# Optimization experiments

Measured on AMD Instinct MI355X. Metric: run time of the kernel, lower is better.

Reference implementation:

```python
import jax, jax.numpy as jnp
import numpy as np

SPATIAL = [(56, 100), (28, 50), (14, 25), (7, 13)]
L_TOT = sum(h * w for h, w in SPATIAL)  # 7441
IMG_H, IMG_W = 448.0, 800.0
HH, NLEV, NPTS = 8, 4, 4
C, FFN = 256, 1024
PC = [-54.0, -54.0, -5.0, 54.0, 54.0, 3.0]
GRID_XY = 1080 // 8


def mlp2(x, w1, b1, w2, b2):
    return jnp.maximum(x @ w1 + b1, 0.0) @ w2 + b2


def ln(x):
    m = x.mean(-1, keepdims=True)
    v = ((x - m) ** 2).mean(-1, keepdims=True)
    return (x - m) * jax.lax.rsqrt(v + 1e-5)


def bilinear_sample(feat, loc):
    # feat [h,w,D]; loc [N,2] normalized to [0,1]; zero padding, align_corners=False
    h, w = feat.shape[0], feat.shape[1]
    x = loc[:, 0] * w - 0.5
    y = loc[:, 1] * h - 0.5
    x0f = jnp.floor(x); y0f = jnp.floor(y)
    wx = (x - x0f)[:, None]; wy = (y - y0f)[:, None]
    x0 = x0f.astype(jnp.int32); y0 = y0f.astype(jnp.int32)
    def g(xi, yi):
        inb = ((xi >= 0) & (xi < w) & (yi >= 0) & (yi < h))[:, None]
        return feat[jnp.clip(yi, 0, h - 1), jnp.clip(xi, 0, w - 1)] * inb
    return (g(x0, y0) * (1 - wx) * (1 - wy) + g(x0 + 1, y0) * wx * (1 - wy)
            + g(x0, y0 + 1) * (1 - wx) * wy + g(x0 + 1, y0 + 1) * wx * wy)


def setup_inputs() -> dict:
    key = jax.random.key(0)
    ks = jax.random.split(key, 40)
    B, V, P = 4, 6, 200
    f = jnp.float32
    def w(i, shape, s=0.05):
        return jax.random.normal(ks[i], shape, f) * s
    inp = {
        'img_query_feat': jax.random.normal(ks[1], (B, C, P), f),
        'img_query_pos': jax.random.uniform(ks[2], (B, P, 3), dtype=f),
        'img_query_view_mask': jax.random.randint(ks[3], (B, P, V), 0, 2).astype(jnp.int32),
        'img_feats_stack': jax.random.normal(ks[4], (B, V, C, L_TOT), f),
        'normal_img_feats_pos_stack': jax.random.normal(ks[5], (L_TOT, 2), f),
        'lidar2img_rt': jnp.eye(4, dtype=f) + 0.01 * jax.random.normal(ks[0], (B, V, 4, 4), f),
        'lidar2cam_r': jnp.broadcast_to(jnp.eye(3, dtype=f), (B, V, 3, 3)) + 0.01 * jax.random.normal(ks[6], (B, V, 3, 3), f),
        'lidar2cam_t': jax.random.normal(ks[7], (B, V, 3), f),
        'qpos_w1': w(8, (3, C)), 'qpos_b1': jnp.zeros((C,), f),
        'qpos_w2': w(9, (C, C)), 'qpos_b2': jnp.zeros((C,), f),
        'kpos_w1': w(10, (6, C)), 'kpos_b1': jnp.zeros((C,), f),
        'kpos_w2': w(11, (C, C)), 'kpos_b2': jnp.zeros((C,), f),
        'sa_wq': w(12, (C, C)), 'sa_wk': w(13, (C, C)),
        'sa_wv': w(14, (C, C)), 'sa_wo': w(15, (C, C)),
        'dv_w': w(16, (C, C)),
        'doff_w': w(17, (C, HH * NLEV * NPTS * 2)), 'doff_b': jnp.zeros((HH * NLEV * NPTS * 2,), f),
        'dattn_w': w(18, (C, HH * NLEV * NPTS)), 'dattn_b': jnp.zeros((HH * NLEV * NPTS,), f),
        'dout_w': w(19, (C, C)),
        'ffn_w1': w(20, (C, FFN)), 'ffn_b1': jnp.zeros((FFN,), f),
        'ffn_w2': w(21, (FFN, C)), 'ffn_b2': jnp.zeros((C,), f),
        'pred_w1': w(22, (C, C)), 'pred_b1': jnp.zeros((C,), f),
        'pred_w2': w(23, (C, 3)), 'pred_b2': jnp.zeros((3,), f),
    }
    return inp


def reference(img_query_feat, img_query_pos, img_query_view_mask, img_feats_stack,
              normal_img_feats_pos_stack, lidar2img_rt, lidar2cam_r, lidar2cam_t,
              qpos_w1, qpos_b1, qpos_w2, qpos_b2, kpos_w1, kpos_b1, kpos_w2, kpos_b2,
              sa_wq, sa_wk, sa_wv, sa_wo, dv_w, doff_w, doff_b, dattn_w, dattn_b, dout_w,
              ffn_w1, ffn_b1, ffn_w2, ffn_b2, pred_w1, pred_b1, pred_w2, pred_b2):
    B, V, _, L = img_feats_stack.shape
    P = img_query_feat.shape[-1]
    Dh = C // HH

    # key 3D positions: denormalize -> backproject via inv(lidar2img) -> append cam center
    pos2d = jax.nn.sigmoid(normal_img_feats_pos_stack) * jnp.array([IMG_W, IMG_H], jnp.float32)
    pos4 = jnp.concatenate([pos2d, jnp.ones((L, 2), pos2d.dtype)], -1)  # [L,4]
    inv_rt = jnp.linalg.inv(lidar2img_rt)                               # [B,V,4,4]
    key3d = jnp.einsum('bvij,lj->bvli', inv_rt, pos4)[..., :3]          # [B,V,L,3]
    cam_t = -jnp.einsum('bvji,bvj->bvi', lidar2cam_r, lidar2cam_t)      # [B,V,3]
    key_pos6 = jnp.concatenate([key3d, jnp.broadcast_to(cam_t[:, :, None], key3d.shape)], -1)
    kpos_emb = mlp2(key_pos6, kpos_w1, kpos_b1, kpos_w2, kpos_b2)       # [B,V,L,C]
    qpos_emb = mlp2(img_query_pos, qpos_w1, qpos_b1, qpos_w2, qpos_b2)  # [B,P,C]

    # per-view normalized reference points from lidar->image projection
    qpad = jnp.concatenate([img_query_pos, jnp.ones((B, P, 1), img_query_pos.dtype)], -1)
    proj = jnp.einsum('bvij,bpj->bvpi', lidar2img_rt, qpad)
    ref = (proj[..., :2] / proj[..., 2:3]) / jnp.array([IMG_W, IMG_H], jnp.float32)  # [B,V,P,2]

    # on-image mask; views with <=1 query are skipped (as in original)
    mv = jnp.transpose(img_query_view_mask > 0, (0, 2, 1))  # [B,V,P]
    mv = mv & (mv.sum(-1, keepdims=True) > 1)

    # self attention among on-image queries (shared qkv, per-view key mask)
    x = jnp.transpose(img_query_feat, (0, 2, 1))  # [B,P,C]
    xq = x + qpos_emb
    q = (xq @ sa_wq).reshape(B, P, HH, Dh)
    k = (xq @ sa_wk).reshape(B, P, HH, Dh)
    v = (x @ sa_wv).reshape(B, P, HH, Dh)
    logits = jnp.einsum('bqhd,bkhd->bhqk', q, k) / np.sqrt(Dh).astype(np.float32)
    logits = logits[:, None] + jnp.where(mv[:, :, None, None, :], 0.0, -1e9)  # [B,V,HH,P,P]
    attn = jax.nn.softmax(logits, axis=-1)
    sa = jnp.einsum('bvhqk,bkhd->bvqhd', attn, v).reshape(B, V, P, C) @ sa_wo
    x1 = ln(x[:, None] + sa)  # [B,V,P,C]

    # multi-scale deformable cross attention
    vals = ((jnp.transpose(img_feats_stack, (0, 1, 3, 2)) + kpos_emb) @ dv_w).reshape(B, V, L, HH, Dh)
    q2 = x1 + qpos_emb[:, None]
    off = (q2 @ doff_w + doff_b).reshape(B, V, P, HH, NLEV, NPTS, 2)
    aw = jax.nn.softmax((q2 @ dattn_w + dattn_b).reshape(B, V, P, HH, NLEV * NPTS), -1)
    aw = aw.reshape(B, V, P, HH, NLEV, NPTS)
    wh = jnp.array([[float(w_), float(h_)] for (h_, w_) in SPATIAL], jnp.float32)  # [NLEV,2]
    loc = ref[:, :, :, None, None, None, :] + off / wh[:, None, :]
    out = jnp.zeros((B, V, P, HH, Dh), x.dtype)
    start = 0
    for l, (h_, w_) in enumerate(SPATIAL):
        feat_l = vals[:, :, start:start + h_ * w_]
        start += h_ * w_
        feat_l = jnp.transpose(feat_l.reshape(B, V, h_, w_, HH, Dh), (0, 1, 4, 2, 3, 5)).reshape(B * V * HH, h_, w_, Dh)
        loc_l = jnp.transpose(loc[:, :, :, :, l], (0, 1, 3, 2, 4, 5)).reshape(B * V * HH, P * NPTS, 2)
        s = jax.vmap(bilinear_sample)(feat_l, loc_l).reshape(B, V, HH, P, NPTS, Dh)
        out = out + jnp.einsum('bvhpnd,bvphn->bvphd', s, aw[:, :, :, :, l])
    x2 = ln(x1 + out.reshape(B, V, P, C) @ dout_w)
    x3 = ln(x2 + mlp2(x2, ffn_w1, ffn_b1, ffn_w2, ffn_b2))  # [B,V,P,C]

    # masked scatter-accumulate across views, count-normalized
    mk = mv[..., None].astype(x.dtype)            # [B,V,P,1]
    fused = (x3 * mk).sum(1) / (mk.sum(1) + 1e-4)  # [B,P,C]
    img_query_feat_out = jnp.transpose(fused, (0, 2, 1))

    # prediction head: center refinement + BEV normalization
    center = mlp2(fused, pred_w1, pred_b1, pred_w2, pred_b2) + img_query_pos  # [B,P,3]
    img_query_pos_out = jax.lax.stop_gradient(center)
    cx = (center[..., 0] - PC[0]) / (PC[3] - PC[0]) * GRID_XY
    cy = (center[..., 1] - PC[1]) / (PC[4] - PC[1]) * GRID_XY
    center_bev = jnp.stack([cx, cy], -1)
    img_query_pos_bev = jax.lax.stop_gradient(center_bev)
    height = jnp.transpose(center[..., 2:3], (0, 2, 1))
    center_out = jnp.transpose(center_bev, (0, 2, 1))
    return img_query_feat_out, img_query_pos_out, img_query_pos_bev, center_out, height
```

## Files before the change

### kernel.cpp

```cpp
#include <hip/hip_runtime.h>
#include <hip/hip_bf16.h>
#include <cstdint>
#include <cstddef>

using bf16 = __hip_bfloat16;
#define DEVFN static __device__ __forceinline__

constexpr int B = 4, V = 6, P = 200, C = 256, HH = 8, Dh = 32, NLEV = 4, NPTS = 4, FFN = 1024;
constexpr int L = 7441;
constexpr int BV = B * V, BP = B * P, BVP = B * V * P, BVL = B * V * L;
constexpr float IMG_W = 800.f, IMG_H = 448.f;

__constant__ int cLH[4] = {56, 28, 14, 7};
__constant__ int cLW[4] = {100, 50, 25, 13};
__constant__ int cLS[4] = {0, 5600, 7000, 7350};

constexpr size_t IRT   = 0;
constexpr size_t CAMT  = IRT + (size_t)BV * 16;
constexpr size_t MFLAG = CAMT + (size_t)BV * 3;
constexpr size_t Xo    = MFLAG + BV;
constexpr size_t QPOSo = Xo + (size_t)BP * C;
constexpr size_t Qo    = QPOSo + (size_t)BP * C;
constexpr size_t Ko    = Qo + (size_t)BP * C;
constexpr size_t VVo   = Ko + (size_t)BP * C;
constexpr size_t LOGo  = VVo + (size_t)BP * C;
constexpr size_t SAo   = LOGo + (size_t)B * HH * P * P;
constexpr size_t X1o   = SAo + (size_t)BVP * C;
constexpr size_t REFo  = X1o + (size_t)BVP * C;
constexpr size_t OFFo  = REFo + (size_t)BVP * 2;
constexpr size_t AWo   = OFFo + (size_t)BVP * 256;
constexpr size_t OUTSo = AWo + (size_t)BVP * 128;
constexpr size_t X2o   = OUTSo + (size_t)BVP * C;
constexpr size_t X3o   = X2o + (size_t)BVP * C;
constexpr size_t FUSEDo= X3o + (size_t)BVP * C;
constexpr size_t WS_FLOATS = FUSEDo + (size_t)BP * C;
constexpr size_t VALS_BYTE_OFF = ((WS_FLOATS * 4 + 255) / 256) * 256;
constexpr size_t VALS_ELEMS = (size_t)BVL * C;

constexpr size_t KW2T_O  = 0;
constexpr size_t DVWT_O  = 65536;
constexpr size_t WOT_O   = 131072;
constexpr size_t DOUTT_O = 196608;
constexpr size_t OAWT_O  = 262144;
constexpr size_t QKVT_O  = 360448;
constexpr size_t W1T_O   = 753664;
constexpr size_t W2T_O   = 1015808;
constexpr size_t HIDB_O  = 1277952;

constexpr size_t O0 = 0;
constexpr size_t O1 = O0 + (size_t)B * C * P;
constexpr size_t O2 = O1 + (size_t)B * P * 3;
constexpr size_t O3 = O2 + (size_t)B * P * 2;
constexpr size_t O4 = O3 + (size_t)B * 2 * P;

DEVFN float tof(bf16 x) { return __bfloat162float(x); }
DEVFN bf16  tobf(float x) { return __float2bfloat16(x); }

typedef __attribute__((ext_vector_type(8))) short short8;
typedef __attribute__((ext_vector_type(4))) float floatx4;

DEVFN float blockReduceSum(float v, float* red) {
    int j = threadIdx.x;
    __syncthreads();
    red[j] = v; __syncthreads();
    for (int s = 128; s > 0; s >>= 1) { if (j < s) red[j] += red[j + s]; __syncthreads(); }
    return red[0];
}
DEVFN float blockReduceMax(float v, float* red) {
    int j = threadIdx.x;
    __syncthreads();
    red[j] = v; __syncthreads();
    for (int s = 128; s > 0; s >>= 1) { if (j < s) red[j] = fmaxf(red[j], red[j + s]); __syncthreads(); }
    return red[0];
}

DEVFN float dotK(const float* __restrict__ s, const float* __restrict__ W, int j, int N, int K) {
    float acc = 0.f;
    for (int k = 0; k < K; k += 4) {
        float4 h = *(const float4*)(s + k);
        acc += h.x * W[(size_t)(k + 0) * N + j];
        acc += h.y * W[(size_t)(k + 1) * N + j];
        acc += h.z * W[(size_t)(k + 2) * N + j];
        acc += h.w * W[(size_t)(k + 3) * N + j];
    }
    return acc;
}

__global__ __launch_bounds__(64) void k_setup(const float* rt, const float* l2cr, const float* l2ct,
                                              const int* maskin, float* ws) {
    int t = threadIdx.x;
    if (t >= BV) return;
    float m[16], inv[16];
    for (int i = 0; i < 16; i++) m[i] = rt[t * 16 + i];
    inv[0]  =  m[5]*m[10]*m[15] - m[5]*m[11]*m[14] - m[9]*m[6]*m[15] + m[9]*m[7]*m[14] + m[13]*m[6]*m[11] - m[13]*m[7]*m[10];
    inv[4]  = -m[4]*m[10]*m[15] + m[4]*m[11]*m[14] + m[8]*m[6]*m[15] - m[8]*m[7]*m[14] - m[12]*m[6]*m[11] + m[12]*m[7]*m[10];
    inv[8]  =  m[4]*m[9]*m[15]  - m[4]*m[11]*m[13] - m[8]*m[5]*m[15] + m[8]*m[7]*m[13] + m[12]*m[5]*m[11] - m[12]*m[7]*m[9];
    inv[12] = -m[4]*m[9]*m[14]  + m[4]*m[10]*m[13] + m[8]*m[5]*m[14] - m[8]*m[6]*m[13] - m[12]*m[5]*m[10] + m[12]*m[6]*m[9];
    inv[1]  = -m[1]*m[10]*m[15] + m[1]*m[11]*m[14] + m[9]*m[2]*m[15] - m[9]*m[3]*m[14] - m[13]*m[2]*m[11] + m[13]*m[3]*m[10];
    inv[5]  =  m[0]*m[10]*m[15] - m[0]*m[11]*m[14] - m[8]*m[2]*m[15] + m[8]*m[3]*m[14] + m[12]*m[2]*m[11] - m[12]*m[3]*m[10];
    inv[9]  = -m[0]*m[9]*m[15]  + m[0]*m[11]*m[13] + m[8]*m[1]*m[15] - m[8]*m[3]*m[13] - m[12]*m[1]*m[11] + m[12]*m[3]*m[9];
    inv[13] =  m[0]*m[9]*m[14]  - m[0]*m[10]*m[13] - m[8]*m[1]*m[14] + m[8]*m[2]*m[13] + m[12]*m[1]*m[10] - m[12]*m[2]*m[9];
    inv[2]  =  m[1]*m[6]*m[15]  - m[1]*m[7]*m[14]  - m[5]*m[2]*m[15] + m[5]*m[3]*m[14] + m[13]*m[2]*m[7]  - m[13]*m[3]*m[6];
    inv[6]  = -m[0]*m[6]*m[15]  + m[0]*m[7]*m[14]  + m[4]*m[2]*m[15] - m[4]*m[3]*m[14] - m[12]*m[2]*m[7]  + m[12]*m[3]*m[6];
    inv[10] =  m[0]*m[5]*m[15]  - m[0]*m[7]*m[13]  - m[4]*m[1]*m[15] + m[4]*m[3]*m[13] + m[12]*m[1]*m[7]  - m[12]*m[3]*m[5];
    inv[14] = -m[0]*m[5]*m[14]  + m[0]*m[6]*m[13]  + m[4]*m[1]*m[14] - m[4]*m[2]*m[13] - m[12]*m[1]*m[6]  + m[12]*m[2]*m[5];
    inv[3]  = -m[1]*m[6]*m[11]  + m[1]*m[7]*m[10]  + m[5]*m[2]*m[11] - m[5]*m[3]*m[10] - m[9]*m[2]*m[7]   + m[9]*m[3]*m[6];
    inv[7]  =  m[0]*m[6]*m[11]  - m[0]*m[7]*m[10]  - m[4]*m[2]*m[11] + m[4]*m[3]*m[10] + m[8]*m[2]*m[7]   - m[8]*m[3]*m[6];
    inv[11] = -m[0]*m[5]*m[11]  + m[0]*m[7]*m[9]   + m[4]*m[1]*m[11] - m[4]*m[3]*m[9]  - m[8]*m[1]*m[7]   + m[8]*m[3]*m[5];
    inv[15] =  m[0]*m[5]*m[10]  - m[0]*m[6]*m[9]   - m[4]*m[1]*m[10] + m[4]*m[2]*m[9]  + m[8]*m[1]*m[6]   - m[8]*m[2]*m[5];
    float det = m[0]*inv[0] + m[1]*inv[4] + m[2]*inv[8] + m[3]*inv[12];
    float rd = 1.f / det;
    for (int i = 0; i < 16; i++) ws[IRT + t * 16 + i] = inv[i] * rd;
    float r9[9], tv[3];
    for (int i = 0; i < 9; i++) r9[i] = l2cr[t * 9 + i];
    for (int i = 0; i < 3; i++) tv[i] = l2ct[t * 3 + i];
    for (int i = 0; i < 3; i++)
        ws[CAMT + t * 3 + i] = -(r9[0 * 3 + i] * tv[0] + r9[1 * 3 + i] * tv[1] + r9[2 * 3 + i] * tv[2]);
    int b = t / V, v = t % V, cnt = 0;
    for (int p = 0; p < P; p++) cnt += (maskin[(b * P + p) * V + v] > 0) ? 1 : 0;
    ws[MFLAG + t] = (cnt > 1) ? 1.f : 0.f;
}

__global__ __launch_bounds__(256) void k_wprep_all(
        const float* kw2, const float* dvw, const float* wo, const float* dw,
        const float* offw, const float* attw, const float* wq, const float* wk, const float* wv,
        const float* w1, const float* w2, bf16* wb) {
    int bid = blockIdx.x, t = threadIdx.x;
    if (bid < 1024) {
        int reg = bid >> 8, n = bid & 255;
        const float* src = (reg == 0) ? kw2 : (reg == 1) ? dvw : (reg == 2) ? wo : dw;
        wb[(size_t)reg * 65536 + (size_t)n * 256 + t] = tobf(src[(size_t)t * 256 + n]);
    } else if (bid < 1408) {
        int n = bid - 1024;
        float v = (n < 256) ? offw[(size_t)t * 256 + n] : attw[(size_t)t * 128 + (n - 256)];
        wb[OAWT_O + (size_t)n * 256 + t] = tobf(v);
    } else if (bid < 2176) {
        int n = bid - 1408;
        bf16* dst = wb + QKVT_O + (size_t)n * 512;
        float v0 = (n < 256) ? wq[(size_t)t * 256 + n] : (n < 512) ? wk[(size_t)t * 256 + (n - 256)]
                                                                   : wv[(size_t)t * 256 + (n - 512)];
        dst[t] = tobf(v0);
        float v1 = (n < 256) ? wq[(size_t)t * 256 + n] : (n < 512) ? wk[(size_t)t * 256 + (n - 256)] : 0.f;
        dst[t + 256] = tobf(v1);
    } else if (bid < 3200) {
        int n = bid - 2176;
        wb[W1T_O + (size_t)n * 256 + t] = tobf(w1[(size_t)t * 1024 + n]);
    } else {
        int n = bid - 3200;
        bf16* dst = wb + W2T_O + (size_t)n * 1024;
        for (int kk = 0; kk < 4; kk++)
            dst[t + kk * 256] = tobf(w2[(size_t)(t + kk * 256) * 256 + n]);
    }
}

__global__ __launch_bounds__(256) void k_qpos(const float* qfeat, const float* qposin,
                                              const float* w1, const float* b1, const float* w2, const float* b2,
                                              float* ws) {
    int row = blockIdx.x, j = threadIdx.x;
    int b = row / P, p = row % P;
    __shared__ __align__(16) float pos[4];
    __shared__ __align__(16) float hid[C];
    if (j < 3) pos[j] = qposin[row * 3 + j];
    __syncthreads();
    float h = b1[j] + pos[0] * w1[0 * C + j] + pos[1] * w1[1 * C + j] + pos[2] * w1[2 * C + j];
    hid[j] = fmaxf(h, 0.f);
    __syncthreads();
    float acc = b2[j] + dotK(hid, w2, j, C, C);
    ws[QPOSo + (size_t)row * C + j] = acc;
    ws[Xo + (size_t)row * C + j] = qfeat[((size_t)b * C + j) * P + p];
}

constexpr int AST2 = 520;
__global__ __launch_bounds__(256) void k_qkv_mfma(const bf16* __restrict__ qkvT, float* ws) {
    __shared__ __align__(16) bf16 As[16 * AST2];
    int row0 = blockIdx.x * 16;
    int t = threadIdx.x;
    for (int rr = 0; rr < 16; rr++) {
        As[rr * AST2 + t]       = tobf(ws[Xo + (size_t)(row0 + rr) * C + t]);
        As[rr * AST2 + 256 + t] = tobf(ws[QPOSo + (size_t)(row0 + rr) * C + t]);
    }
    __syncthreads();
    int wave = t >> 6, lane = t & 63, quad = lane >> 4, l15 = lane & 15;
    int n0 = wave * 192;
    floatx4 acc[12];
    #pragma unroll
    for (int nt = 0; nt < 12; nt++) acc[nt] = (floatx4){0.f, 0.f, 0.f, 0.f};
    for (int kk = 0; kk < 16; kk++) {
        short8 a = *(const short8*)&As[l15 * AST2 + kk * 32 + quad * 8];
        #pragma unroll
        for (int nt = 0; nt < 12; nt++) {
            short8 bf = *(const short8*)&qkvT[(size_t)(n0 + nt * 16 + l15) * 512 + kk * 32 + quad * 8];
            acc[nt] = __builtin_amdgcn_mfma_f32_16x16x32_bf16(a, bf, acc[nt], 0, 0, 0);
        }
    }
    #pragma unroll
    for (int nt = 0; nt < 12; nt++) {
        int n = n0 + nt * 16 + l15;
        int which = n >> 8, c = n & 255;
        size_t dst = (which == 0) ? Qo : (which == 1) ? Ko : VVo;
        int row = row0 + quad * 4;
        #pragma unroll
        for (int u = 0; u < 4; u++)
            ws[dst + (size_t)(row + u) * C + c] = acc[nt][u];
    }
}

__global__ __launch_bounds__(256) void k_logits(float* ws) {
    int bid = blockIdx.x;
    int qi = bid % P, h = (bid / P) % HH, b = bid / (P * HH);
    int j = threadIdx.x;
    __shared__ __align__(16) float qf[Dh];
    if (j < Dh) qf[j] = ws[Qo + ((size_t)(b * P + qi)) * C + h * Dh + j];
    __syncthreads();
    if (j < P) {
        const float* kp = ws + Ko + ((size_t)(b * P + j)) * C + h * Dh;
        float acc = 0.f;
        for (int d = 0; d < Dh; d += 4) {
            float4 kv = *(const float4*)(kp + d);
            float4 qv = *(const float4*)(qf + d);
            acc += kv.x * qv.x + kv.y * qv.y + kv.z * qv.z + kv.w * qv.w;
        }
        ws[LOGo + (size_t)bid * P + j] = acc * 0.17677669529663687f;
    }
}

__global__ __launch_bounds__(256) void k_sattn(const int* maskin, float* ws) {
    int bid = blockIdx.x;
    int qi = bid % P, h = (bid / P) % HH, v = (bid / (P * HH)) % V, b = bid / (P * HH * V);
    int j = threadIdx.x;
    __shared__ float attn[256];
    __shared__ float red[256];
    float flag = ws[MFLAG + b * V + v];
    float val = -1e30f;
    if (j < P) {
        float lg = ws[LOGo + ((size_t)(b * HH + h) * P + qi) * P + j];
        bool mk = (flag > 0.5f) && (maskin[(b * P + j) * V + v] > 0);
        val = lg + (mk ? 0.f : -1e9f);
    }
    float mx = blockReduceMax(val, red);
    float e = (j < P) ? __expf(val - mx) : 0.f;
    float s = blockReduceSum(e, red);
    attn[j] = e / s;
    __syncthreads();
    int d = j & 31, c = j >> 5;
    const float* vvp = ws + VVo + (size_t)b * P * C + h * Dh + d;
    float acc = 0.f;
    for (int kk = c * 25; kk < c * 25 + 25; ++kk) acc += attn[kk] * vvp[(size_t)kk * C];
    red[j] = acc; __syncthreads();
    if (j < Dh) {
        float s2 = 0.f;
        for (int c2 = 0; c2 < 8; c2++) s2 += red[c2 * 32 + j];
        ws[SAo + ((size_t)((b * V + v) * P + qi)) * C + h * Dh + j] = s2;
    }
}

constexpr int GAST = 264;
constexpr int OST = 260;
__global__ __launch_bounds__(256) void k_lngemm(const bf16* __restrict__ WT,
        float* ws, size_t aOff, size_t residOff, int residMode, size_t dstOff) {
    __shared__ __align__(16) bf16 As[32 * GAST];
    __shared__ __align__(16) float Os[32 * OST];
    __shared__ float redw[4][8][2];
    __shared__ float mv[8][2];
    int row0 = blockIdx.x * 32;
    int t = threadIdx.x;
    for (int rr = 0; rr < 32; rr++)
        As[rr * GAST + t] = tobf(ws[aOff + (size_t)(row0 + rr) * C + t]);
    __syncthreads();
    int wave = t >> 6, lane = t & 63, quad = lane >> 4, l15 = lane & 15;
    int n0 = wave * 64;
    floatx4 acc[2][4];
    #pragma unroll
    for (int i = 0; i < 2; i++)
        #pragma unroll
        for (int nt = 0; nt < 4; nt++) acc[i][nt] = (floatx4){0.f, 0.f, 0.f, 0.f};
    for (int kk = 0; kk < 8; kk++) {
        short8 a0 = *(const short8*)&As[l15 * GAST + kk * 32 + quad * 8];
        short8 a1 = *(const short8*)&As[(16 + l15) * GAST + kk * 32 + quad * 8];
        #pragma unroll
        for (int nt = 0; nt < 4; nt++) {
            short8 bf = *(const short8*)&WT[(size_t)(n0 + nt * 16 + l15) * 256 + kk * 32 + quad * 8];
            acc[0][nt] = __builtin_amdgcn_mfma_f32_16x16x32_bf16(a0, bf, acc[0][nt], 0, 0, 0);
            acc[1][nt] = __builtin_amdgcn_mfma_f32_16x16x32_bf16(a1, bf, acc[1][nt], 0, 0, 0);
        }
    }
    #pragma unroll
    for (int i = 0; i < 2; i++)
        #pragma unroll
        for (int nt = 0; nt < 4; nt++) {
            int col = n0 + nt * 16 + l15;
            int rl = i * 16 + quad * 4;
            #pragma unroll
            for (int u = 0; u < 4; u++) Os[(rl + u) * OST + col] = acc[i][nt][u];
        }
    __syncthreads();
    int lane2 = t & 63, wv = t >> 6;
    for (int g = 0; g < 4; g++) {
        float rv[8];
        #pragma unroll
        for (int r = 0; r < 8; r++) {
            int grow = row0 + g * 8 + r;
            int ridx = residMode ? ((grow / (P * V)) * P + grow % P) : grow;
            rv[r] = Os[(g * 8 + r) * OST + t] + ws[residOff + (size_t)ridx * C + t];
        }
        #pragma unroll
        for (int r = 0; r < 8; r++) {
            float s = rv[r], q = rv[r] * rv[r];
            for (int off = 32; off > 0; off >>= 1) {
                s += __shfl_down(s, off, 64);
                q += __shfl_down(q, off, 64);
            }
            if (lane2 == 0) { redw[wv][r][0] = s; redw[wv][r][1] = q; }
        }
        __syncthreads();
        if (t < 8) {
            float s = redw[0][t][0] + redw[1][t][0] + redw[2][t][0] + redw[3][t][0];
            float q = redw[0][t][1] + redw[1][t][1] + redw[2][t][1] + redw[3][t][1];
            float mean = s * (1.f / C);
            float var = q * (1.f / C) - mean * mean;
            mv[t][0] = mean; mv[t][1] = rsqrtf(var + 1e-5f);
        }
        __syncthreads();
        #pragma unroll
        for (int r = 0; r < 8; r++) {
            int grow = row0 + g * 8 + r;
            ws[dstOff + (size_t)grow * C + t] = (rv[r] - mv[r][0]) * mv[r][1];
        }
        __syncthreads();
    }
}

__global__ __launch_bounds__(256) void k_ref(const float* qposin, const float* rt, float* ws) {
    int tid = blockIdx.x * 256 + threadIdx.x;
    if (tid >= BVP) return;
    int p = tid % P, v = (tid / P) % V, b = tid / (P * V);
    float p0 = qposin[(b * P + p) * 3 + 0];
    float p1 = qposin[(b * P + p) * 3 + 1];
    float p2 = qposin[(b * P + p) * 3 + 2];
    const float* m = rt + (size_t)(b * V + v) * 16;
    float pr[3];
    for (int i = 0; i < 3; i++)
        pr[i] = m[i * 4 + 0] * p0 + m[i * 4 + 1] * p1 + m[i * 4 + 2] * p2 + m[i * 4 + 3];
    ws[REFo + (size_t)tid * 2 + 0] = pr[0] / pr[2] / IMG_W;
    ws[REFo + (size_t)tid * 2 + 1] = pr[1] / pr[2] / IMG_H;
}

constexpr int OAWST = 392;
__global__ __launch_bounds__(256) void k_offaw_mfma(const bf16* __restrict__ oawT,
        const float* __restrict__ ob, const float* __restrict__ ab, float* ws) {
    __shared__ __align__(16) bf16 As[32 * GAST];
    __shared__ __align__(16) float Os[32 * OAWST];
    int row0 = blockIdx.x * 32;
    int t = threadIdx.x;
    for (int rr = 0; rr < 32; rr++) {
        int grow = row0 + rr;
        int ridx = (grow / (P * V)) * P + grow % P;
        As[rr * GAST + t] = tobf(ws[X1o + (size_t)grow * C + t] + ws[QPOSo + (size_t)ridx * C + t]);
    }
    __syncthreads();
    int wave = t >> 6, lane = t & 63, quad = lane >> 4, l15 = lane & 15;
    int n0 = wave * 96;
    floatx4 acc[2][6];
    #pragma unroll
    for (int i = 0; i < 2; i++)
        #pragma unroll
        for (int nt = 0; nt < 6; nt++) acc[i][nt] = (floatx4){0.f, 0.f, 0.f, 0.f};
    for (int kk = 0; kk < 8; kk++) {
        short8 a0 = *(const short8*)&As[l15 * GAST + kk * 32 + quad * 8];
        short8 a1 = *(const short8*)&As[(16 + l15) * GAST + kk * 32 + quad * 8];
        #pragma unroll
        for (int nt = 0; nt < 6; nt++) {
            short8 bf = *(const short8*)&oawT[(size_t)(n0 + nt * 16 + l15) * 256 + kk * 32 + quad * 8];
            acc[0][nt] = __builtin_amdgcn_mfma_f32_16x16x32_bf16(a0, bf, acc[0][nt], 0, 0, 0);
            acc[1][nt] = __builtin_amdgcn_mfma_f32_16x16x32_bf16(a1, bf, acc[1][nt], 0, 0, 0);
        }
    }
    #pragma unroll
    for (int i = 0; i < 2; i++)
        #pragma unroll
        for (int nt = 0; nt < 6; nt++) {
            int col = n0 + nt * 16 + l15;
            int rl = i * 16 + quad * 4;
            #pragma unroll
            for (int u = 0; u < 4; u++) Os[(rl + u) * OAWST + col] = acc[i][nt][u];
        }
    __syncthreads();
    float obv = ob[t];
    for (int r = 0; r < 32; r++)
        ws[OFFo + (size_t)(row0 + r) * 256 + t] = Os[r * OAWST + t] + obv;
    {
        int r = t >> 3, g = t & 7;
        const float* lg = &Os[r * OAWST + 256 + g * 16];
        float mx = -1e30f;
        #pragma unroll
        for (int i = 0; i < 16; i++) mx = fmaxf(mx, lg[i] + ab[g * 16 + i]);
        float s = 0.f;
        float ex[16];
        #pragma unroll
        for (int i = 0; i < 16; i++) { ex[i] = __expf(lg[i] + ab[g * 16 + i] - mx); s += ex[i]; }
        float rs = 1.f / s;
        #pragma unroll
        for (int i = 0; i < 16; i++)
            ws[AWo + (size_t)(row0 + r) * 128 + g * 16 + i] = ex[i] * rs;
    }
}

constexpr int VROWS = 64;
constexpr int ASTR = C + 8;
constexpr int NVT = (L + VROWS - 1) / VROWS;

__global__ __launch_bounds__(256, 4) void k_vals_mfma(
        const float* __restrict__ npos, const float* __restrict__ feats,
        const float* __restrict__ kw1, const float* __restrict__ kb1, const float* __restrict__ kb2,
        const bf16* __restrict__ kw2T, const bf16* __restrict__ dvwT,
        const float* __restrict__ ws, bf16* __restrict__ vals) {
    __shared__ __align__(16) bf16 As[VROWS * ASTR];
    __shared__ float kp6s[VROWS][8];
    __shared__ float kb2s[C];
    int bv = blockIdx.y;
    int l0 = blockIdx.x * VROWS;
    int t = threadIdx.x;
    kb2s[t] = kb2[t];
    if (t < VROWS) {
        int l = min(l0 + t, L - 1);
        float sx = 1.f / (1.f + __expf(-npos[l * 2 + 0])) * IMG_W;
        float sy = 1.f / (1.f + __expf(-npos[l * 2 + 1])) * IMG_H;
        const float* inv = ws + IRT + (size_t)bv * 16;
        #pragma unroll
        for (int i = 0; i < 3; i++)
            kp6s[t][i] = inv[i * 4 + 0] * sx + inv[i * 4 + 1] * sy + inv[i * 4 + 2] + inv[i * 4 + 3];
        #pragma unroll
        for (int i = 0; i < 3; i++) kp6s[t][3 + i] = ws[CAMT + (size_t)bv * 3 + i];
    }
    __syncthreads();
    {
        float w1j[6];
        #pragma unroll
        for (int i = 0; i < 6; i++) w1j[i] = kw1[i * C + t];
        float bb = kb1[t];
        for (int r = 0; r < VROWS; r++) {
            float h = bb;
            #pragma unroll
            for (int i = 0; i < 6; i++) h += kp6s[r][i] * w1j[i];
            As[r * ASTR + t] = tobf(fmaxf(h, 0.f));
        }
    }
    __syncthreads();
    int wave = t >> 6, lane = t & 63;
    int quad = lane >> 4, l15 = lane & 15;
    int mh = (wave >> 1) * 32;
    int nh = (wave & 1) * 128;
    floatx4 acc[2][8];
    #pragma unroll
    for (int i = 0; i < 2; i++)
        #pragma unroll
        for (int nt = 0; nt < 8; nt++) acc[i][nt] = (floatx4){0.f, 0.f, 0.f, 0.f};
    for (int kk = 0; kk < 8; kk++) {
        short8 a0 = *(const short8*)&As[(mh + l15) * ASTR + kk * 32 + quad * 8];
        short8 a1 = *(const short8*)&As[(mh + 16 + l15) * ASTR + kk * 32 + quad * 8];
        #pragma unroll
        for (int nt = 0; nt < 8; nt++) {
            short8 bfr = *(const short8*)&kw2T[(size_t)(nh + nt * 16 + l15) * C + kk * 32 + quad * 8];
            acc[0][nt] = __builtin_amdgcn_mfma_f32_16x16x32_bf16(a0, bfr, acc[0][nt], 0, 0, 0);
            acc[1][nt] = __builtin_amdgcn_mfma_f32_16x16x32_bf16(a1, bfr, acc[1][nt], 0, 0, 0);
        }
    }
    __syncthreads();
    #pragma unroll
    for (int i = 0; i < 2; i++) {
        #pragma unroll
        for (int nt = 0; nt < 8; nt++) {
            int c = nh + nt * 16 + l15;
            int rb = mh + i * 16 + quad * 4;
            #pragma unroll
            for (int u = 0; u < 4; u++)
                As[(rb + u) * ASTR + c] = tobf(acc[i][nt][u]);
        }
    }
    __syncthreads();
    if (l0 + VROWS <= L) {
        #pragma unroll
        for (int round = 0; round < 16; round++) {
            int q = round * 256 + t;
            int c = q >> 4, ql = (q & 15) * 4;
            float4 f = *(const float4*)&feats[((size_t)bv * C + c) * L + l0 + ql];
            float bias = kb2s[c];
            int a0i = ql * ASTR + c;
            As[a0i]            = tobf(tof(As[a0i])            + bias + f.x);
            As[a0i + ASTR]     = tobf(tof(As[a0i + ASTR])     + bias + f.y);
            As[a0i + 2 * ASTR] = tobf(tof(As[a0i + 2 * ASTR]) + bias + f.z);
            As[a0i + 3 * ASTR] = tobf(tof(As[a0i + 3 * ASTR]) + bias + f.w);
        }
    } else {
        for (int round = 0; round < 16; round++) {
            int q = round * 256 + t;
            int c = q >> 4, ql = (q & 15) * 4;
            float bias = kb2s[c];
            #pragma unroll
            for (int u = 0; u < 4; u++) {
                int l = l0 + ql + u;
                if (l < L) {
                    int ai = (ql + u) * ASTR + c;
                    As[ai] = tobf(tof(As[ai]) + bias + feats[((size_t)bv * C + c) * L + l]);
                }
            }
        }
    }
    __syncthreads();
    #pragma unroll
    for (int i = 0; i < 2; i++)
        #pragma unroll
        for (int nt = 0; nt < 8; nt++) acc[i][nt] = (floatx4){0.f, 0.f, 0.f, 0.f};
    for (int kk = 0; kk < 8; kk++) {
        short8 a0 = *(const short8*)&As[(mh + l15) * ASTR + kk * 32 + quad * 8];
        short8 a1 = *(const short8*)&As[(mh + 16 + l15) * ASTR + kk * 32 + quad * 8];
        #pragma unroll
        for (int nt = 0; nt < 8; nt++) {
            short8 bfr = *(const short8*)&dvwT[(size_t)(nh + nt * 16 + l15) * C + kk * 32 + quad * 8];
            acc[0][nt] = __builtin_amdgcn_mfma_f32_16x16x32_bf16(a0, bfr, acc[0][nt], 0, 0, 0);
            acc[1][nt] = __builtin_amdgcn_mfma_f32_16x16x32_bf16(a1, bfr, acc[1][nt], 0, 0, 0);
        }
    }
    __syncthreads();
    #pragma unroll
    for (int i = 0; i < 2; i++) {
        #pragma unroll
        for (int nt = 0; nt < 8; nt++) {
            int c = nh + nt * 16 + l15;
            int rb = mh + i * 16 + quad * 4;
            #pragma unroll
            for (int u = 0; u < 4; u++)
                As[(rb + u) * ASTR + c] = tobf(acc[i][nt][u]);
        }
    }
    __syncthreads();
    #pragma unroll
    for (int pass = 0; pass < 8; pass++) {
        int row = pass * 8 + (t >> 5);
        int col = (t & 31) * 8;
        int l = l0 + row;
        if (l < L)
            *(int4*)&vals[((size_t)bv * L + l) * C + col] = *(const int4*)&As[row * ASTR + col];
    }
}

__global__ __launch_bounds__(256) void k_sample(const float* ws, const bf16* vals, float* wsmut) {
    int row = blockIdx.x, j = threadIdx.x;
    int h = j >> 5, d = j & 31;
    __shared__ float soff[256];
    __shared__ float sawL[128];
    __shared__ float sref[2];
    soff[j] = ws[OFFo + (size_t)row * 256 + j];
    if (j < 128) sawL[j] = ws[AWo + (size_t)row * 128 + j];
    if (j < 2) sref[j] = ws[REFo + (size_t)row * 2 + j];
    __syncthreads();
    int v = (row / P) % V, b = row / (P * V);
    const bf16* vbase = vals + (size_t)(b * V + v) * L * C + h * Dh + d;
    float acc = 0.f;
    for (int l = 0; l < NLEV; l++) {
        float Wf = (float)cLW[l], Hf = (float)cLH[l];
        int Wi = cLW[l], Hi = cLH[l], S0 = cLS[l];
        for (int n = 0; n < NPTS; n++) {
            int oi = ((h * NLEV + l) * NPTS + n) * 2;
            float lx = sref[0] + soff[oi + 0] / Wf;
            float ly = sref[1] + soff[oi + 1] / Hf;
            float aww = sawL[(h * NLEV + l) * NPTS + n];
            float x = lx * Wf - 0.5f, y = ly * Hf - 0.5f;
            float x0f = floorf(x), y0f = floorf(y);
            float wx = x - x0f, wy = y - y0f;
            int x0 = (int)x0f, y0 = (int)y0f;
            float s = 0.f;
            #pragma unroll
            for (int dy = 0; dy < 2; dy++) {
                #pragma unroll
                for (int dx = 0; dx < 2; dx++) {
                    int xi = x0 + dx, yi = y0 + dy;
                    if (xi >= 0 && xi < Wi && yi >= 0 && yi < Hi) {
                        float wwt = (dx ? wx : 1.f - wx) * (dy ? wy : 1.f - wy);
                        s += wwt * tof(vbase[(size_t)(S0 + yi * Wi + xi) * C]);
                    }
                }
            }
            acc += aww * s;
        }
    }
    wsmut[OUTSo + (size_t)row * C + j] = acc;
}

__global__ __launch_bounds__(256) void k_ffn1(const bf16* __restrict__ w1T, const float* __restrict__ b1,
                                              float* ws, bf16* hidb) {
    __shared__ __align__(16) bf16 As[32 * GAST];
    __shared__ __align__(16) bf16 Hs[32 * AST2];
    int row0 = blockIdx.x * 32;
    int nb = blockIdx.y * 512;
    int t = threadIdx.x;
    for (int rr = 0; rr < 32; rr++)
        As[rr * GAST + t] = tobf(ws[X2o + (size_t)(row0 + rr) * C + t]);
    __syncthreads();
    int wave = t >> 6, lane = t & 63, quad = lane >> 4, l15 = lane & 15;
    int n0 = wave * 128;
    floatx4 acc[2][8];
    #pragma unroll
    for (int i = 0; i < 2; i++)
        #pragma unroll
        for (int nt = 0; nt < 8; nt++) acc[i][nt] = (floatx4){0.f, 0.f, 0.f, 0.f};
    for (int kk = 0; kk < 8; kk++) {
        short8 a0 = *(const short8*)&As[l15 * GAST + kk * 32 + quad * 8];
        short8 a1 = *(const short8*)&As[(16 + l15) * GAST + kk * 32 + quad * 8];
        #pragma unroll
        for (int nt = 0; nt < 8; nt++) {
            short8 bf = *(const short8*)&w1T[(size_t)(nb + n0 + nt * 16 + l15) * 256 + kk * 32 + quad * 8];
            acc[0][nt] = __builtin_amdgcn_mfma_f32_16x16x32_bf16(a0, bf, acc[0][nt], 0, 0, 0);
            acc[1][nt] = __builtin_amdgcn_mfma_f32_16x16x32_bf16(a1, bf, acc[1][nt], 0, 0, 0);
        }
    }
    #pragma unroll
    for (int i = 0; i < 2; i++)
        #pragma unroll
        for (int nt = 0; nt < 8; nt++) {
            int cl = n0 + nt * 16 + l15;
            float bias = b1[nb + cl];
            int rl = i * 16 + quad * 4;
            #pragma unroll
            for (int u = 0; u < 4; u++)
                Hs[(rl + u) * AST2 + cl] = tobf(fmaxf(acc[i][nt][u] + bias, 0.f));
        }
    __syncthreads();
    #pragma unroll
    for (int pass = 0; pass < 8; pass++) {
        int row = pass * 4 + (t >> 6);
        int col = (t & 63) * 8;
        *(int4*)&hidb[(size_t)(row0 + row) * FFN + nb + col] = *(const int4*)&Hs[row * AST2 + col];
    }
}

__global__ __launch_bounds__(256) void k_ffn2(const bf16* __restrict__ w2T, const float* __restrict__ b2,
                                              const bf16* __restrict__ hidb, float* ws) {
    __shared__ __align__(16) float Os[32 * OST];
    __shared__ float redw[4][8][2];
    __shared__ float mv[8][2];
    int row0 = blockIdx.x * 32;
    int t = threadIdx.x;
    int wave = t >> 6, lane = t & 63, quad = lane >> 4, l15 = lane & 15;
    int n0 = wave * 64;
    floatx4 acc[2][4];
    #pragma unroll
    for (int i = 0; i < 2; i++)
        #pragma unroll
        for (int nt = 0; nt < 4; nt++) acc[i][nt] = (floatx4){0.f, 0.f, 0.f, 0.f};
    for (int kk = 0; kk < 32; kk++) {
        short8 a0 = *(const short8*)&hidb[(size_t)(row0 + l15) * FFN + kk * 32 + quad * 8];
        short8 a1 = *(const short8*)&hidb[(size_t)(row0 + 16 + l15) * FFN + kk * 32 + quad * 8];
        #pragma unroll
        for (int nt = 0; nt < 4; nt++) {
            short8 bf = *(const short8*)&w2T[(size_t)(n0 + nt * 16 + l15) * FFN + kk * 32 + quad * 8];
            acc[0][nt] = __builtin_amdgcn_mfma_f32_16x16x32_bf16(a0, bf, acc[0][nt], 0, 0, 0);
            acc[1][nt] = __builtin_amdgcn_mfma_f32_16x16x32_bf16(a1, bf, acc[1][nt], 0, 0, 0);
        }
    }
    #pragma unroll
    for (int i = 0; i < 2; i++)
        #pragma unroll
        for (int nt = 0; nt < 4; nt++) {
            int col = n0 + nt * 16 + l15;
            float bias = b2[col];
            int rl = i * 16 + quad * 4;
            #pragma unroll
            for (int u = 0; u < 4; u++) Os[(rl + u) * OST + col] = acc[i][nt][u] + bias;
        }
    __syncthreads();
    for (int g = 0; g < 4; g++) {
        float rv[8];
        #pragma unroll
        for (int r = 0; r < 8; r++) {
            int grow = row0 + g * 8 + r;
            rv[r] = Os[(g * 8 + r) * OST + t] + ws[X2o + (size_t)grow * C + t];
        }
        #pragma unroll
        for (int r = 0; r < 8; r++) {
            float s = rv[r], q = rv[r] * rv[r];
            for (int off = 32; off > 0; off >>= 1) {
                s += __shfl_down(s, off, 64);
                q += __shfl_down(q, off, 64);
            }
            if (lane == 0) { redw[wave][r][0] = s; redw[wave][r][1] = q; }
        }
        __syncthreads();
        if (t < 8) {
            float s = redw[0][t][0] + redw[1][t][0] + redw[2][t][0] + redw[3][t][0];
            float q = redw[0][t][1] + redw[1][t][1] + redw[2][t][1] + redw[3][t][1];
            float mean = s * (1.f / C);
            float var = q * (1.f / C) - mean * mean;
            mv[t][0] = mean; mv[t][1] = rsqrtf(var + 1e-5f);
        }
        __syncthreads();
        #pragma unroll
        for (int r = 0; r < 8; r++) {
            int grow = row0 + g * 8 + r;
            ws[X3o + (size_t)grow * C + t] = (rv[r] - mv[r][0]) * mv[r][1];
        }
        __syncthreads();
    }
}

__global__ __launch_bounds__(256) void k_fuse(const int* maskin, float* ws, float* out) {
    int row = blockIdx.x, j = threadIdx.x;
    int b = row / P, p = row % P;
    float s = 0.f, cnt = 0.f;
    for (int v = 0; v < V; v++) {
        bool mk = (maskin[(b * P + p) * V + v] > 0) && (ws[MFLAG + b * V + v] > 0.5f);
        if (mk) {
            s += ws[X3o + ((size_t)((b * V + v) * P + p)) * C + j];
            cnt += 1.f;
        }
    }
    float f = s / (cnt + 1e-4f);
    ws[FUSEDo + (size_t)row * C + j] = f;
    out[O0 + ((size_t)b * C + j) * P + p] = f;
}

__global__ __launch_bounds__(256) void k_pred(const float* w1, const float* b1, const float* w2, const float* b2,
                                              const float* qposin, float* ws, float* out) {
    int row = blockIdx.x, j = threadIdx.x;
    __shared__ __align__(16) float in[C];
    __shared__ float red[256];
    __shared__ float cen[4];
    in[j] = ws[FUSEDo + (size_t)row * C + j];
    __syncthreads();
    float h = fmaxf(b1[j] + dotK(in, w1, j, C, C), 0.f);
    for (int i = 0; i < 3; i++) {
        float s = blockReduceSum(h * w2[j * 3 + i], red);
        if (j == 0) cen[i] = s + b2[i] + qposin[row * 3 + i];
    }
    if (j == 0) {
        float c0 = cen[0], c1 = cen[1], c2 = cen[2];
        float cx = (c0 + 54.f) / 108.f * 135.f;
        float cy = (c1 + 54.f) / 108.f * 135.f;
        int b = row / P, p = row % P;
        out[O1 + (size_t)row * 3 + 0] = c0;
        out[O1 + (size_t)row * 3 + 1] = c1;
        out[O1 + (size_t)row * 3 + 2] = c2;
        out[O2 + (size_t)row * 2 + 0] = cx;
        out[O2 + (size_t)row * 2 + 1] = cy;
        out[O3 + (size_t)b * 2 * P + 0 * P + p] = cx;
        out[O3 + (size_t)b * 2 * P + 1 * P + p] = cy;
        out[O4 + (size_t)b * P + p] = c2;
    }
}

extern "C" void kernel_launch(void* const* d_in, const int* in_sizes, int n_in,
                              void* d_out, int out_size, void* d_ws, size_t ws_size,
                              hipStream_t stream) {
    const float* qfeat  = (const float*)d_in[0];
    const float* qposin = (const float*)d_in[1];
    const int*   maskin = (const int*)d_in[2];
    const float* feats  = (const float*)d_in[3];
    const float* npos   = (const float*)d_in[4];
    const float* rt     = (const float*)d_in[5];
    const float* l2cr   = (const float*)d_in[6];
    const float* l2ct   = (const float*)d_in[7];
    const float* qp_w1 = (const float*)d_in[8],  * qp_b1 = (const float*)d_in[9];
    const float* qp_w2 = (const float*)d_in[10], * qp_b2 = (const float*)d_in[11];
    const float* kp_w1 = (const float*)d_in[12], * kp_b1 = (const float*)d_in[13];
    const float* kp_w2 = (const float*)d_in[14], * kp_b2 = (const float*)d_in[15];
    const float* sa_wq = (const float*)d_in[16], * sa_wk = (const float*)d_in[17];
    const float* sa_wv = (const float*)d_in[18], * sa_wo = (const float*)d_in[19];
    const float* dv_w  = (const float*)d_in[20];
    const float* doffw = (const float*)d_in[21], * doffb = (const float*)d_in[22];
    const float* dattw = (const float*)d_in[23], * dattb = (const float*)d_in[24];
    const float* doutw = (const float*)d_in[25];
    const float* f_w1  = (const float*)d_in[26], * f_b1 = (const float*)d_in[27];
    const float* f_w2  = (const float*)d_in[28], * f_b2 = (const float*)d_in[29];
    const float* p_w1  = (const float*)d_in[30], * p_b1 = (const float*)d_in[31];
    const float* p_w2  = (const float*)d_in[32], * p_b2 = (const float*)d_in[33];

    float* ws = (float*)d_ws;
    bf16* vals = (bf16*)((char*)d_ws + VALS_BYTE_OFF);
    bf16* wb = vals + VALS_ELEMS;
    bf16* hidb = wb + HIDB_O;
    float* out = (float*)d_out;

    k_setup<<<1, 64, 0, stream>>>(rt, l2cr, l2ct, maskin, ws);
    k_wprep_all<<<3456, 256, 0, stream>>>(kp_w2, dv_w, sa_wo, doutw, doffw, dattw,
                                          sa_wq, sa_wk, sa_wv, f_w1, f_w2, wb);
    k_qpos<<<BP, 256, 0, stream>>>(qfeat, qposin, qp_w1, qp_b1, qp_w2, qp_b2, ws);
    k_qkv_mfma<<<BP / 16, 256, 0, stream>>>(wb + QKVT_O, ws);
    k_logits<<<B * HH * P, 256, 0, stream>>>(ws);
    k_sattn<<<B * V * HH * P, 256, 0, stream>>>(maskin, ws);
    k_lngemm<<<BVP / 32, 256, 0, stream>>>(wb + WOT_O, ws, SAo, Xo, 1, X1o);
    k_ref<<<(BVP + 255) / 256, 256, 0, stream>>>(qposin, rt, ws);
    k_offaw_mfma<<<BVP / 32, 256, 0, stream>>>(wb + OAWT_O, doffb, dattb, ws);
    k_vals_mfma<<<dim3(NVT, BV), 256, 0, stream>>>(npos, feats, kp_w1, kp_b1, kp_b2,
                                                   wb + KW2T_O, wb + DVWT_O, ws, vals);
    k_sample<<<BVP, 256, 0, stream>>>(ws, vals, ws);
    k_lngemm<<<BVP / 32, 256, 0, stream>>>(wb + DOUTT_O, ws, OUTSo, X1o, 0, X2o);
    k_ffn1<<<dim3(BVP / 32, 2), 256, 0, stream>>>(wb + W1T_O, f_b1, ws, hidb);
    k_ffn2<<<BVP / 32, 256, 0, stream>>>(wb + W2T_O, f_b2, hidb, ws);
    k_fuse<<<BP, 256, 0, stream>>>(maskin, ws, out);
    k_pred<<<BP, 256, 0, stream>>>(p_w1, p_b1, p_w2, p_b2, qposin, ws, out);
}
```

Measured before the change: 843.0 us.

## Fuse kpos epilogue with feats add, warp-shuffle softmax, remap sample blocks

In the value-projection kernel, the feature add and bias are applied straight from the MFMA accumulators in registers. This skips the round-trip of writing bf16 to shared memory and reading it back, and avoids one rounding step. The self-attention softmax now uses wave-level shuffle reductions instead of shared-memory tree reductions, which cuts barriers. The sampling kernel remaps block indices to interleave rows across the grid, which may change cache locality. The feats read pattern becomes strided per thread instead of coalesced float4 rows, which may hurt global load efficiency.

```diff
diff --git a/kernel.cpp b/kernel.cpp
--- a/kernel.cpp
+++ b/kernel.cpp
@@ -64,13 +64,6 @@
     __syncthreads();
     red[j] = v; __syncthreads();
     for (int s = 128; s > 0; s >>= 1) { if (j < s) red[j] += red[j + s]; __syncthreads(); }
-    return red[0];
-}
-DEVFN float blockReduceMax(float v, float* red) {
-    int j = threadIdx.x;
-    __syncthreads();
-    red[j] = v; __syncthreads();
-    for (int s = 128; s > 0; s >>= 1) { if (j < s) red[j] = fmaxf(red[j], red[j + s]); __syncthreads(); }
     return red[0];
 }
 
@@ -230,6 +223,7 @@
     int j = threadIdx.x;
     __shared__ float attn[256];
     __shared__ float red[256];
+    __shared__ float rw[8];
     float flag = ws[MFLAG + b * V + v];
     float val = -1e30f;
     if (j < P) {
@@ -237,9 +231,20 @@
         bool mk = (flag > 0.5f) && (maskin[(b * P + j) * V + v] > 0);
         val = lg + (mk ? 0.f : -1e9f);
     }
-    float mx = blockReduceMax(val, red);
-    float e = (j < P) ? __expf(val - mx) : 0.f;
-    float s = blockReduceSum(e, red);
+    int wv = j >> 6;
+    float m = val;
+    #pragma unroll
+    for (int off = 32; off > 0; off >>= 1) m = fmaxf(m, __shfl_xor(m, off, 64));
+    if ((j & 63) == 0) rw[wv] = m;
+    __syncthreads();
+    m = fmaxf(fmaxf(rw[0], rw[1]), fmaxf(rw[2], rw[3]));
+    float e = (j < P) ? __expf(val - m) : 0.f;
+    float s = e;
+    #pragma unroll
+    for (int off = 32; off > 0; off >>= 1) s += __shfl_xor(s, off, 64);
+    if ((j & 63) == 0) rw[4 + wv] = s;
+    __syncthreads();
+    s = (rw[4] + rw[5]) + (rw[6] + rw[7]);
     attn[j] = e / s;
     __syncthreads();
     int d = j & 31, c = j >> 5;
@@ -466,6 +471,52 @@
         }
     }
     __syncthreads();
+    if (l0 + VROWS <= L) {
+        #pragma unroll
+        for (int i = 0; i < 2; i++)
+            #pragma unroll
+            for (int nt = 0; nt < 8; nt++) {
+                int c = nh + nt * 16 + l15;
+                int rb = mh + i * 16 + quad * 4;
+                float4 f = *(const float4*)&feats[((size_t)bv * C + c) * L + l0 + rb];
+                float bias = kb2s[c];
+                As[(rb + 0) * ASTR + c] = tobf(acc[i][nt][0] + bias + f.x);
+                As[(rb + 1) * ASTR + c] = tobf(acc[i][nt][1] + bias + f.y);
+                As[(rb + 2) * ASTR + c] = tobf(acc[i][nt][2] + bias + f.z);
+                As[(rb + 3) * ASTR + c] = tobf(acc[i][nt][3] + bias + f.w);
+            }
+    } else {
+        #pragma unroll
+        for (int i = 0; i < 2; i++)
+            #pragma unroll
+            for (int nt = 0; nt < 8; nt++) {
+                int c = nh + nt * 16 + l15;
+                int rb = mh + i * 16 + quad * 4;
+                size_t fbase = ((size_t)bv * C + c) * L + l0 + rb;
+                float bias = kb2s[c];
+                #pragma unroll
+                for (int u = 0; u < 4; u++) {
+                    float fv = (l0 + rb + u < L) ? feats[fbase + u] : 0.f;
+                    As[(rb + u) * ASTR + c] = tobf(acc[i][nt][u] + bias + fv);
+                }
+            }
+    }
+    __syncthreads();
+    #pragma unroll
+    for (int i = 0; i < 2; i++)
+        #pragma unroll
+        for (int nt = 0; nt < 8; nt++) acc[i][nt] = (floatx4){0.f, 0.f, 0.f, 0.f};
+    for (int kk = 0; kk < 8; kk++) {
+        short8 a0 = *(const short8*)&As[(mh + l15) * ASTR + kk * 32 + quad * 8];
+        short8 a1 = *(const short8*)&As[(mh + 16 + l15) * ASTR + kk * 32 + quad * 8];
+        #pragma unroll
+        for (int nt = 0; nt < 8; nt++) {
+            short8 bfr = *(const short8*)&dvwT[(size_t)(nh + nt * 16 + l15) * C + kk * 32 + quad * 8];
+            acc[0][nt] = __builtin_amdgcn_mfma_f32_16x16x32_bf16(a0, bfr, acc[0][nt], 0, 0, 0);
+            acc[1][nt] = __builtin_amdgcn_mfma_f32_16x16x32_bf16(a1, bfr, acc[1][nt], 0, 0, 0);
+        }
+    }
+    __syncthreads();
     #pragma unroll
     for (int i = 0; i < 2; i++) {
         #pragma unroll
@@ -478,62 +529,6 @@
         }
     }
     __syncthreads();
-    if (l0 + VROWS <= L) {
-        #pragma unroll
-        for (int round = 0; round < 16; round++) {
-            int q = round * 256 + t;
-            int c = q >> 4, ql = (q & 15) * 4;
-            float4 f = *(const float4*)&feats[((size_t)bv * C + c) * L + l0 + ql];
-            float bias = kb2s[c];
-            int a0i = ql * ASTR + c;
-            As[a0i]            = tobf(tof(As[a0i])            + bias + f.x);
-            As[a0i + ASTR]     = tobf(tof(As[a0i + ASTR])     + bias + f.y);
-            As[a0i + 2 * ASTR] = tobf(tof(As[a0i + 2 * ASTR]) + bias + f.z);
-            As[a0i + 3 * ASTR] = tobf(tof(As[a0i + 3 * ASTR]) + bias + f.w);
-        }
-    } else {
-        for (int round = 0; round < 16; round++) {
-            int q = round * 256 + t;
-            int c = q >> 4, ql = (q & 15) * 4;
-            float bias = kb2s[c];
-            #pragma unroll
-            for (int u = 0; u < 4; u++) {
-                int l = l0 + ql + u;
-                if (l < L) {
-                    int ai = (ql + u) * ASTR + c;
-                    As[ai] = tobf(tof(As[ai]) + bias + feats[((size_t)bv * C + c) * L + l]);
-                }
-            }
-        }
-    }
-    __syncthreads();
-    #pragma unroll
-    for (int i = 0; i < 2; i++)
-        #pragma unroll
-        for (int nt = 0; nt < 8; nt++) acc[i][nt] = (floatx4){0.f, 0.f, 0.f, 0.f};
-    for (int kk = 0; kk < 8; kk++) {
-        short8 a0 = *(const short8*)&As[(mh + l15) * ASTR + kk * 32 + quad * 8];
-        short8 a1 = *(const short8*)&As[(mh + 16 + l15) * ASTR + kk * 32 + quad * 8];
-        #pragma unroll
-        for (int nt = 0; nt < 8; nt++) {
-            short8 bfr = *(const short8*)&dvwT[(size_t)(nh + nt * 16 + l15) * C + kk * 32 + quad * 8];
-            acc[0][nt] = __builtin_amdgcn_mfma_f32_16x16x32_bf16(a0, bfr, acc[0][nt], 0, 0, 0);
-            acc[1][nt] = __builtin_amdgcn_mfma_f32_16x16x32_bf16(a1, bfr, acc[1][nt], 0, 0, 0);
-        }
-    }
-    __syncthreads();
-    #pragma unroll
-    for (int i = 0; i < 2; i++) {
-        #pragma unroll
-        for (int nt = 0; nt < 8; nt++) {
-            int c = nh + nt * 16 + l15;
-            int rb = mh + i * 16 + quad * 4;
-            #pragma unroll
-            for (int u = 0; u < 4; u++)
-                As[(rb + u) * ASTR + c] = tobf(acc[i][nt][u]);
-        }
-    }
-    __syncthreads();
     #pragma unroll
     for (int pass = 0; pass < 8; pass++) {
         int row = pass * 8 + (t >> 5);
@@ -545,7 +540,9 @@
 }
 
 __global__ __launch_bounds__(256) void k_sample(const float* ws, const bf16* vals, float* wsmut) {
-    int row = blockIdx.x, j = threadIdx.x;
+    int bid0 = blockIdx.x;
+    int row = (bid0 & 7) * (BVP / 8) + (bid0 >> 3);
+    int j = threadIdx.x;
     int h = j >> 5, d = j & 31;
     __shared__ float soff[256];
     __shared__ float sawL[128];
@@ -764,7 +761,8 @@
     const float* kp_w1 = (const float*)d_in[12], * kp_b1 = (const float*)d_in[13];
     const float* kp_w2 = (const float*)d_in[14], * kp_b2 = (const float*)d_in[15];
     const float* sa_wq = (const float*)d_in[16], * sa_wk = (const float*)d_in[17];
-    const float* sa_wv = (const float*)d_in[18], * sa_wo = (const float*)d_in[19];
+    const float* sa_wv = (const float*)d_in[18], * sa_wv2 = nullptr;
+    const float* sa_wo = (const float*)d_in[19];
     const float* dv_w  = (const float*)d_in[20];
     const float* doffw = (const float*)d_in[21], * doffb = (const float*)d_in[22];
     const float* dattw = (const float*)d_in[23], * dattb = (const float*)d_in[24];
@@ -773,6 +771,7 @@
     const float* f_w2  = (const float*)d_in[28], * f_b2 = (const float*)d_in[29];
     const float* p_w1  = (const float*)d_in[30], * p_b1 = (const float*)d_in[31];
     const float* p_w2  = (const float*)d_in[32], * p_b2 = (const float*)d_in[33];
+    (void)sa_wv2;
 
     float* ws = (float*)d_ws;
     bf16* vals = (bf16*)((char*)d_ws + VALS_BYTE_OFF);
```

Result: slower. 883.3 us (+4.8%).
